# Kernel tuning notes

Hardware: AMD Instinct MI355X
Metric: run time of the kernel (lower is better)

The kernel has to match this reference:

```python
import jax, jax.numpy as jnp
import numpy as np

N_NODES = 100000
N_EDGES = 1600000

def _graph_conv(x, src, dst, W_rel, b_rel, W_root):
    # sum-aggregate source features at destination nodes (PyG GraphConv, aggr='add')
    agg = jax.ops.segment_sum(x[src], dst, num_segments=N_NODES)  # [N, Fin]
    return agg @ W_rel.T + b_rel + x @ W_root.T  # [N, Fout]

def setup_inputs() -> dict:
    key = jax.random.key(0)
    ks = jax.random.split(key, 10)
    x = jax.random.normal(ks[0], (N_NODES, 4), dtype=jnp.float32)
    edge_index = jax.random.randint(ks[1], (2, N_EDGES), 0, N_NODES, dtype=jnp.int32)
    def lin(k, fo, fi):
        return jax.random.normal(k, (fo, fi), dtype=jnp.float32) / np.sqrt(fi)
    return {
        "x": x,
        "edge_index": edge_index,
        "W1_rel": lin(ks[2], 128, 4),
        "b1": jax.random.normal(ks[3], (128,), dtype=jnp.float32) * 0.01,
        "W1_root": lin(ks[4], 128, 4),
        "W2_rel": lin(ks[5], 128, 128),
        "b2": jax.random.normal(ks[6], (128,), dtype=jnp.float32) * 0.01,
        "W2_root": lin(ks[7], 128, 128),
        "Wlin": lin(ks[8], 2, 128),
        "blin": jax.random.normal(ks[9], (2,), dtype=jnp.float32) * 0.01,
    }

def reference(x, edge_index, W1_rel, b1, W1_root, W2_rel, b2, W2_root, Wlin, blin):
    src, dst = edge_index[0], edge_index[1]
    h = jax.nn.relu(_graph_conv(x, src, dst, W1_rel, b1, W1_root))   # [N,128]
    h = jax.nn.relu(_graph_conv(h, src, dst, W2_rel, b2, W2_root))   # [N,128]
    # global_mean_pool with batch = zeros -> mean over all nodes, single graph
    g = jnp.mean(h, axis=0, keepdims=True)                           # [1,128]
    return g @ Wlin.T + blin                                         # [1,2]
```

## Files before the change

kernel.cpp:

```cpp
#include <hip/hip_runtime.h>
#include <cstddef>

#define N_NODES 100000
#define N_EDGES 1600000
#define NCHUNK32 3125
#define BUCK_SHIFT 6
#define BUCK_NODES 64
#define NBUCK 1563
#define EB_CAP 1536
#define BF_EDGES 4096
#define BF_BLOCKS ((N_EDGES + BF_EDGES - 1) / BF_EDGES)

typedef __attribute__((ext_vector_type(8))) short short8;
typedef __attribute__((ext_vector_type(4))) float f32x4;
typedef __attribute__((ext_vector_type(2))) float f32x2;

__device__ __forceinline__ unsigned pack_bf16x2(float a, float b) {
  unsigned ua = __float_as_uint(a); ua += 0x7FFFu + ((ua >> 16) & 1u);
  unsigned ub = __float_as_uint(b); ub += 0x7FFFu + ((ub >> 16) & 1u);
  return (ua >> 16) | (ub & 0xFFFF0000u);
}

__global__ __launch_bounds__(512) void k_init(int* __restrict__ bucket_cursor,
                                              float* __restrict__ gsum,
                                              const float* __restrict__ W2_rel,
                                              const float* __restrict__ W2_root,
                                              unsigned* __restrict__ wbuf) {
  int t = threadIdx.x;
  for (int b = t; b < NBUCK; b += 512) bucket_cursor[b] = b * EB_CAP;
  if (t < 128) gsum[t] = 0.0f;
#pragma unroll
  for (int i = 0; i < 8; ++i) {
    int e = t + i * 512;
    int L = e & 63, T = (e >> 6) & 7, K0 = e >> 9;
    int f = T * 16 + (L & 15);
    int k0 = K0 * 32 + ((L >> 4) << 3);
    const float* wsrc = (k0 < 128) ? (W2_rel + f * 128 + k0)
                                   : (W2_root + f * 128 + (k0 - 128));
    float4 w0 = *(const float4*)(wsrc);
    float4 w1 = *(const float4*)(wsrc + 4);
    unsigned* d = wbuf + e * 4;
    d[0] = pack_bf16x2(w0.x, w0.y);
    d[1] = pack_bf16x2(w0.z, w0.w);
    d[2] = pack_bf16x2(w1.x, w1.y);
    d[3] = pack_bf16x2(w1.z, w1.w);
  }
}

__global__ __launch_bounds__(256) void k_bfill(const int* __restrict__ src,
                                               const int* __restrict__ dst,
                                               int* __restrict__ bucket_cursor,
                                               unsigned* __restrict__ ebuf) {
  __shared__ int lh[NBUCK];
  __shared__ int sub_base[NBUCK];
  __shared__ int cur[NBUCK];
  int t = threadIdx.x;
  for (int b = t; b < NBUCK; b += 256) { lh[b] = 0; cur[b] = 0; }
  __syncthreads();
  int e0 = blockIdx.x * BF_EDGES;
  unsigned pk[16];
  int bk[16];
#pragma unroll
  for (int i = 0; i < 16; ++i) {
    int e = e0 + i * 256 + t;
    bk[i] = -1;
    if (e < N_EDGES) {
      int d = dst[e];
      int b = d >> BUCK_SHIFT;
      bk[i] = b;
      pk[i] = ((unsigned)(d & (BUCK_NODES - 1)) << 17) | (unsigned)src[e];
      atomicAdd(&lh[b], 1);
    }
  }
  __syncthreads();
  for (int b = t; b < NBUCK; b += 256)
    sub_base[b] = (lh[b] > 0) ? atomicAdd(&bucket_cursor[b], lh[b]) : 0;
  __syncthreads();
#pragma unroll
  for (int i = 0; i < 16; ++i) {
    if (bk[i] >= 0) {
      int pos = sub_base[bk[i]] + atomicAdd(&cur[bk[i]], 1);
      if (pos < (bk[i] + 1) * EB_CAP) ebuf[pos] = pk[i];
    }
  }
}

__global__ __launch_bounds__(256) void k_fill2(
    const unsigned* __restrict__ ebuf, const int* __restrict__ bucket_cursor,
    const float* __restrict__ x, const float* __restrict__ W1_rel,
    const float* __restrict__ b1, const float* __restrict__ W1_root,
    int* __restrict__ row_start, int* __restrict__ row_end,
    int* __restrict__ csr_src, unsigned* __restrict__ h1b,
    unsigned short* __restrict__ h1f8) {
  __shared__ int cnt[BUCK_NODES];
  __shared__ int start[BUCK_NODES];
  __shared__ float sagg[BUCK_NODES * 4];
  __shared__ float sx[BUCK_NODES * 4];
  __shared__ float sWa[8 * 128];
  __shared__ float sb1[128];
  int t = threadIdx.x;
  int b = blockIdx.x;
  int base = b * EB_CAP;
  int nb = bucket_cursor[b] - base;
  if (nb > EB_CAP) nb = EB_CAP;
  int n0 = b << BUCK_SHIFT;

  if (t < 128) {
    float4 wr = *(const float4*)(W1_rel + t * 4);
    float4 wo = *(const float4*)(W1_root + t * 4);
    sWa[0 * 128 + t] = wr.x; sWa[1 * 128 + t] = wr.y;
    sWa[2 * 128 + t] = wr.z; sWa[3 * 128 + t] = wr.w;
    sWa[4 * 128 + t] = wo.x; sWa[5 * 128 + t] = wo.y;
    sWa[6 * 128 + t] = wo.z; sWa[7 * 128 + t] = wo.w;
    sb1[t] = b1[t];
  }
  sagg[t] = 0.0f;
  if (t < BUCK_NODES) {
    cnt[t] = 0;
    float4 xv = make_float4(0.f, 0.f, 0.f, 0.f);
    if (n0 + t < N_NODES) xv = *(const float4*)(x + (size_t)(n0 + t) * 4);
    *(float4*)&sx[t * 4] = xv;
  }
  __syncthreads();

  for (int i = t; i < nb; i += 256) atomicAdd(&cnt[ebuf[base + i] >> 17], 1);
  __syncthreads();
  if (t == 0) {
    int s = 0;
#pragma unroll
    for (int j = 0; j < BUCK_NODES; ++j) { start[j] = s; s += cnt[j]; }
  }
  __syncthreads();
  if (t < BUCK_NODES) {
    if (n0 + t < N_NODES) row_start[n0 + t] = base + start[t];
    cnt[t] = start[t];
  }
  __syncthreads();
  for (int i = t; i < nb; i += 256) {
    unsigned e = ebuf[base + i];
    int dloc = e >> 17;
    int s = (int)(e & 0x1FFFFu);
    int p = atomicAdd(&cnt[dloc], 1);
    csr_src[base + p] = s;
    float4 v = *(const float4*)(x + (size_t)s * 4);
    atomicAdd(&sagg[dloc * 4 + 0], v.x);
    atomicAdd(&sagg[dloc * 4 + 1], v.y);
    atomicAdd(&sagg[dloc * 4 + 2], v.z);
    atomicAdd(&sagg[dloc * 4 + 3], v.w);
  }
  __syncthreads();
  if (t < BUCK_NODES && n0 + t < N_NODES) row_end[n0 + t] = base + cnt[t];

  for (int it = t; it < BUCK_NODES * 64; it += 256) {
    int nd = it >> 6;
    if (n0 + nd >= N_NODES) break;
    int fp = it & 63;
    int f = fp * 2;
    float4 a  = *(float4*)&sagg[nd * 4];
    float4 xv = *(float4*)&sx[nd * 4];
    float v0 = sb1[f]
        + a.x  * sWa[0 * 128 + f] + a.y  * sWa[1 * 128 + f]
        + a.z  * sWa[2 * 128 + f] + a.w  * sWa[3 * 128 + f]
        + xv.x * sWa[4 * 128 + f] + xv.y * sWa[5 * 128 + f]
        + xv.z * sWa[6 * 128 + f] + xv.w * sWa[7 * 128 + f];
    int f1 = f + 1;
    float v1 = sb1[f1]
        + a.x  * sWa[0 * 128 + f1] + a.y  * sWa[1 * 128 + f1]
        + a.z  * sWa[2 * 128 + f1] + a.w  * sWa[3 * 128 + f1]
        + xv.x * sWa[4 * 128 + f1] + xv.y * sWa[5 * 128 + f1]
        + xv.z * sWa[6 * 128 + f1] + xv.w * sWa[7 * 128 + f1];
    float r0 = fmaxf(v0, 0.f), r1 = fmaxf(v1, 0.f);
    size_t idx = (size_t)(n0 + nd) * 64 + fp;
    h1b[idx] = pack_bf16x2(r0, r1);
    h1f8[idx] = (unsigned short)__builtin_amdgcn_cvt_pk_fp8_f32(r0, r1, 0, false);
  }
}

__global__ __launch_bounds__(256) void k_pull128(
    const unsigned short* __restrict__ h1f8, const int* __restrict__ row_start,
    const int* __restrict__ row_end, const int* __restrict__ csr_src,
    unsigned* __restrict__ agg2b) {
  int w = (blockIdx.x * 256 + threadIdx.x) >> 6;
  if (w >= N_NODES) return;
  int lane = threadIdx.x & 63;
  int rs = row_start[w], re = row_end[w];
  float ax = 0.f, ay = 0.f;
  for (int chunk = rs; chunk < re; chunk += 64) {
    int nv = min(64, re - chunk);
    int sv = (chunk + lane < re) ? csr_src[chunk + lane] : 0;
    int j = 0;
    for (; j + 4 <= nv; j += 4) {
      int s0 = __shfl(sv, j);
      int s1 = __shfl(sv, j + 1);
      int s2 = __shfl(sv, j + 2);
      int s3 = __shfl(sv, j + 3);
      int u0 = h1f8[(size_t)s0 * 64 + lane];
      int u1 = h1f8[(size_t)s1 * 64 + lane];
      int u2 = h1f8[(size_t)s2 * 64 + lane];
      int u3 = h1f8[(size_t)s3 * 64 + lane];
      f32x2 d0 = __builtin_amdgcn_cvt_pk_f32_fp8(u0, false);
      f32x2 d1 = __builtin_amdgcn_cvt_pk_f32_fp8(u1, false);
      f32x2 d2 = __builtin_amdgcn_cvt_pk_f32_fp8(u2, false);
      f32x2 d3 = __builtin_amdgcn_cvt_pk_f32_fp8(u3, false);
      ax += d0.x + d1.x + d2.x + d3.x;
      ay += d0.y + d1.y + d2.y + d3.y;
    }
    for (; j < nv; ++j) {
      int s0 = __shfl(sv, j);
      int u0 = h1f8[(size_t)s0 * 64 + lane];
      f32x2 d0 = __builtin_amdgcn_cvt_pk_f32_fp8(u0, false);
      ax += d0.x; ay += d0.y;
    }
  }
  agg2b[(size_t)w * 64 + lane] = pack_bf16x2(ax, ay);
}

__global__ __launch_bounds__(256) void k_gemm_pool(
    const unsigned* __restrict__ agg2b_u, const unsigned* __restrict__ h1b_u,
    const unsigned* __restrict__ wbuf_u, const float* __restrict__ b2,
    float* __restrict__ gsum) {
  __shared__ float lgs[128];
  int t = threadIdx.x;
  if (t < 128) lgs[t] = 0.0f;
  __syncthreads();

  int lane = t & 63;
  int gw = blockIdx.x * 4 + (t >> 6);
  int lrow = lane & 15;
  int quad = lane >> 4;
  const unsigned short* agg2b = (const unsigned short*)agg2b_u;
  const unsigned short* h1b   = (const unsigned short*)h1b_u;
  const short8* wb = (const short8*)wbuf_u;

  float bias[8];
#pragma unroll
  for (int tt = 0; tt < 8; ++tt) bias[tt] = b2[tt * 16 + lrow];
  float csum[8] = {0.f, 0.f, 0.f, 0.f, 0.f, 0.f, 0.f, 0.f};

  if (gw < NCHUNK32) {
    int mbase = gw * 32;

    f32x4 acc[2][8];
#pragma unroll
    for (int mt = 0; mt < 2; ++mt)
#pragma unroll
      for (int tt = 0; tt < 8; ++tt) acc[mt][tt] = (f32x4){0.f, 0.f, 0.f, 0.f};

#pragma unroll
    for (int ks = 0; ks < 8; ++ks) {
      const unsigned short* abase = (ks < 4)
          ? (agg2b + ks * 32 + quad * 8)
          : (h1b + (ks - 4) * 32 + quad * 8);
      short8 afr[2];
#pragma unroll
      for (int mt = 0; mt < 2; ++mt)
        afr[mt] = *(const short8*)(abase + (size_t)(mbase + mt * 16 + lrow) * 128);
      short8 bfr[8];
#pragma unroll
      for (int tt = 0; tt < 8; ++tt) bfr[tt] = wb[(ks * 8 + tt) * 64 + lane];
#pragma unroll
      for (int mt = 0; mt < 2; ++mt)
#pragma unroll
        for (int tt = 0; tt < 8; ++tt)
          acc[mt][tt] = __builtin_amdgcn_mfma_f32_16x16x32_bf16(
              afr[mt], bfr[tt], acc[mt][tt], 0, 0, 0);
    }

#pragma unroll
    for (int mt = 0; mt < 2; ++mt) {
#pragma unroll
      for (int tt = 0; tt < 8; ++tt) {
        f32x4 v = acc[mt][tt];
        float s = fmaxf(v.x + bias[tt], 0.f) + fmaxf(v.y + bias[tt], 0.f)
                + fmaxf(v.z + bias[tt], 0.f) + fmaxf(v.w + bias[tt], 0.f);
        s += __shfl_xor(s, 16);
        s += __shfl_xor(s, 32);
        csum[tt] += s;
      }
    }
  }
  if (lane < 16) {
#pragma unroll
    for (int tt = 0; tt < 8; ++tt) atomicAdd(&lgs[tt * 16 + lane], csum[tt]);
  }
  __syncthreads();
  if (t < 128) atomicAdd(&gsum[t], lgs[t]);
}

__global__ void k_final(const float* __restrict__ gsum, const float* __restrict__ Wlin,
                        const float* __restrict__ blin, float* __restrict__ out) {
  int lane = threadIdx.x;
  float g0 = gsum[lane];
  float g1 = gsum[lane + 64];
  float s0 = g0 * Wlin[lane]       + g1 * Wlin[lane + 64];
  float s1 = g0 * Wlin[128 + lane] + g1 * Wlin[192 + lane];
#pragma unroll
  for (int off = 32; off > 0; off >>= 1) {
    s0 += __shfl_down(s0, off);
    s1 += __shfl_down(s1, off);
  }
  if (lane == 0) {
    const float inv = 1.0f / (float)N_NODES;
    out[0] = s0 * inv + blin[0];
    out[1] = s1 * inv + blin[1];
  }
}

extern "C" void kernel_launch(void* const* d_in, const int* in_sizes, int n_in,
                              void* d_out, int out_size, void* d_ws, size_t ws_size,
                              hipStream_t stream) {
  const float* x       = (const float*)d_in[0];
  const int*   ei      = (const int*)d_in[1];
  const float* W1_rel  = (const float*)d_in[2];
  const float* b1      = (const float*)d_in[3];
  const float* W1_root = (const float*)d_in[4];
  const float* W2_rel  = (const float*)d_in[5];
  const float* b2      = (const float*)d_in[6];
  const float* W2_root = (const float*)d_in[7];
  const float* Wlin    = (const float*)d_in[8];
  const float* blin    = (const float*)d_in[9];
  const int* src = ei;
  const int* dst = ei + N_EDGES;
  float* out = (float*)d_out;

  char* ws = (char*)d_ws;
  int*            row_start     = (int*)(ws);
  int*            row_end       = (int*)(ws + 400000);
  int*            bucket_cursor = (int*)(ws + 800000);
  float*          gsum          = (float*)(ws + 808192);
  unsigned*       wbuf          = (unsigned*)(ws + 808704);
  int*            csr_src       = (int*)(ws + 874240);
  unsigned*       ebuf          = (unsigned*)(ws + 10477312);
  unsigned*       h1b           = (unsigned*)(ws + 20080384);
  unsigned short* h1f8          = (unsigned short*)(ws + 45680384);
  unsigned*       agg2b         = (unsigned*)(ws + 58480384);

  k_init <<<1, 512, 0, stream>>>(bucket_cursor, gsum, W2_rel, W2_root, wbuf);
  k_bfill<<<BF_BLOCKS, 256, 0, stream>>>(src, dst, bucket_cursor, ebuf);
  k_fill2<<<NBUCK, 256, 0, stream>>>(ebuf, bucket_cursor, x, W1_rel, b1, W1_root,
                                     row_start, row_end, csr_src, h1b, h1f8);
  k_pull128<<<(N_NODES * 64 + 255) / 256, 256, 0, stream>>>(h1f8, row_start, row_end,
                                                            csr_src, agg2b);
  k_gemm_pool<<<(NCHUNK32 + 3) / 4, 256, 0, stream>>>(agg2b, h1b, wbuf, b2, gsum);
  k_final<<<1, 64, 0, stream>>>(gsum, Wlin, blin, out);
}
```

Baseline: 246.9 us.

## Drop bf16 h1 copy, use fp8 root operand, and restructure bucket fill

```diff
diff --git a/kernel.cpp b/kernel.cpp
--- a/kernel.cpp
+++ b/kernel.cpp
@@ -8,7 +8,7 @@
 #define BUCK_NODES 64
 #define NBUCK 1563
 #define EB_CAP 1536
-#define BF_EDGES 4096
+#define BF_EDGES 8192
 #define BF_BLOCKS ((N_EDGES + BF_EDGES - 1) / BF_EDGES)
 
 typedef __attribute__((ext_vector_type(8))) short short8;
@@ -47,7 +47,7 @@
   }
 }
 
-__global__ __launch_bounds__(256) void k_bfill(const int* __restrict__ src,
+__global__ __launch_bounds__(512) void k_bfill(const int* __restrict__ src,
                                                const int* __restrict__ dst,
                                                int* __restrict__ bucket_cursor,
                                                unsigned* __restrict__ ebuf) {
@@ -55,14 +55,14 @@
   __shared__ int sub_base[NBUCK];
   __shared__ int cur[NBUCK];
   int t = threadIdx.x;
-  for (int b = t; b < NBUCK; b += 256) { lh[b] = 0; cur[b] = 0; }
+  for (int b = t; b < NBUCK; b += 512) { lh[b] = 0; cur[b] = 0; }
   __syncthreads();
   int e0 = blockIdx.x * BF_EDGES;
   unsigned pk[16];
   int bk[16];
 #pragma unroll
   for (int i = 0; i < 16; ++i) {
-    int e = e0 + i * 256 + t;
+    int e = e0 + i * 512 + t;
     bk[i] = -1;
     if (e < N_EDGES) {
       int d = dst[e];
@@ -73,7 +73,7 @@
     }
   }
   __syncthreads();
-  for (int b = t; b < NBUCK; b += 256)
+  for (int b = t; b < NBUCK; b += 512)
     sub_base[b] = (lh[b] > 0) ? atomicAdd(&bucket_cursor[b], lh[b]) : 0;
   __syncthreads();
 #pragma unroll
@@ -90,8 +90,7 @@
     const float* __restrict__ x, const float* __restrict__ W1_rel,
     const float* __restrict__ b1, const float* __restrict__ W1_root,
     int* __restrict__ row_start, int* __restrict__ row_end,
-    int* __restrict__ csr_src, unsigned* __restrict__ h1b,
-    unsigned short* __restrict__ h1f8) {
+    int* __restrict__ csr_src, unsigned short* __restrict__ h1f8) {
   __shared__ int cnt[BUCK_NODES];
   __shared__ int start[BUCK_NODES];
   __shared__ float sagg[BUCK_NODES * 4];
@@ -114,7 +113,6 @@
     sWa[6 * 128 + t] = wo.z; sWa[7 * 128 + t] = wo.w;
     sb1[t] = b1[t];
   }
-  sagg[t] = 0.0f;
   if (t < BUCK_NODES) {
     cnt[t] = 0;
     float4 xv = make_float4(0.f, 0.f, 0.f, 0.f);
@@ -125,31 +123,47 @@
 
   for (int i = t; i < nb; i += 256) atomicAdd(&cnt[ebuf[base + i] >> 17], 1);
   __syncthreads();
-  if (t == 0) {
-    int s = 0;
-#pragma unroll
-    for (int j = 0; j < BUCK_NODES; ++j) { start[j] = s; s += cnt[j]; }
-  }
-  __syncthreads();
-  if (t < BUCK_NODES) {
-    if (n0 + t < N_NODES) row_start[n0 + t] = base + start[t];
-    cnt[t] = start[t];
+  if (t < 64) {
+    int v = cnt[t];
+    int incl = v;
+#pragma unroll
+    for (int off = 1; off < 64; off <<= 1) {
+      int nvv = __shfl_up(incl, off);
+      if (t >= off) incl += nvv;
+    }
+    int excl = incl - v;
+    start[t] = excl;
+    cnt[t] = excl;
+    if (n0 + t < N_NODES) row_start[n0 + t] = base + excl;
   }
   __syncthreads();
   for (int i = t; i < nb; i += 256) {
     unsigned e = ebuf[base + i];
-    int dloc = e >> 17;
-    int s = (int)(e & 0x1FFFFu);
-    int p = atomicAdd(&cnt[dloc], 1);
-    csr_src[base + p] = s;
-    float4 v = *(const float4*)(x + (size_t)s * 4);
-    atomicAdd(&sagg[dloc * 4 + 0], v.x);
-    atomicAdd(&sagg[dloc * 4 + 1], v.y);
-    atomicAdd(&sagg[dloc * 4 + 2], v.z);
-    atomicAdd(&sagg[dloc * 4 + 3], v.w);
-  }
-  __syncthreads();
-  if (t < BUCK_NODES && n0 + t < N_NODES) row_end[n0 + t] = base + cnt[t];
+    int p = atomicAdd(&cnt[e >> 17], 1);
+    csr_src[base + p] = (int)(e & 0x1FFFFu);
+  }
+  __syncthreads();
+  {
+    int nd = t >> 2, sub = t & 3;
+    int rs = base + start[nd];
+    int re = base + cnt[nd];
+    float4 acc = make_float4(0.f, 0.f, 0.f, 0.f);
+    for (int i = rs + sub; i < re; i += 4) {
+      int s = csr_src[i];
+      float4 v = *(const float4*)(x + (size_t)s * 4);
+      acc.x += v.x; acc.y += v.y; acc.z += v.z; acc.w += v.w;
+    }
+#pragma unroll
+    for (int off = 1; off < 4; off <<= 1) {
+      acc.x += __shfl_xor(acc.x, off);
+      acc.y += __shfl_xor(acc.y, off);
+      acc.z += __shfl_xor(acc.z, off);
+      acc.w += __shfl_xor(acc.w, off);
+    }
+    if (sub == 0) *(float4*)&sagg[nd * 4] = acc;
+    if (t < 64 && n0 + t < N_NODES) row_end[n0 + t] = base + cnt[t];
+  }
+  __syncthreads();
 
   for (int it = t; it < BUCK_NODES * 64; it += 256) {
     int nd = it >> 6;
@@ -170,9 +184,8 @@
         + xv.x * sWa[4 * 128 + f1] + xv.y * sWa[5 * 128 + f1]
         + xv.z * sWa[6 * 128 + f1] + xv.w * sWa[7 * 128 + f1];
     float r0 = fmaxf(v0, 0.f), r1 = fmaxf(v1, 0.f);
-    size_t idx = (size_t)(n0 + nd) * 64 + fp;
-    h1b[idx] = pack_bf16x2(r0, r1);
-    h1f8[idx] = (unsigned short)__builtin_amdgcn_cvt_pk_fp8_f32(r0, r1, 0, false);
+    h1f8[(size_t)(n0 + nd) * 64 + fp] =
+        (unsigned short)__builtin_amdgcn_cvt_pk_fp8_f32(r0, r1, 0, false);
   }
 }
 
@@ -216,7 +229,7 @@
 }
 
 __global__ __launch_bounds__(256) void k_gemm_pool(
-    const unsigned* __restrict__ agg2b_u, const unsigned* __restrict__ h1b_u,
+    const unsigned* __restrict__ agg2b_u, const unsigned short* __restrict__ h1f8,
     const unsigned* __restrict__ wbuf_u, const float* __restrict__ b2,
     float* __restrict__ gsum) {
   __shared__ float lgs[128];
@@ -229,7 +242,7 @@
   int lrow = lane & 15;
   int quad = lane >> 4;
   const unsigned short* agg2b = (const unsigned short*)agg2b_u;
-  const unsigned short* h1b   = (const unsigned short*)h1b_u;
+  const unsigned char* h8 = (const unsigned char*)h1f8;
   const short8* wb = (const short8*)wbuf_u;
 
   float bias[8];
@@ -247,14 +260,41 @@
       for (int tt = 0; tt < 8; ++tt) acc[mt][tt] = (f32x4){0.f, 0.f, 0.f, 0.f};
 
 #pragma unroll
-    for (int ks = 0; ks < 8; ++ks) {
-      const unsigned short* abase = (ks < 4)
-          ? (agg2b + ks * 32 + quad * 8)
-          : (h1b + (ks - 4) * 32 + quad * 8);
+    for (int ks = 0; ks < 4; ++ks) {
+      const unsigned short* abase = agg2b + ks * 32 + quad * 8;
       short8 afr[2];
 #pragma unroll
       for (int mt = 0; mt < 2; ++mt)
         afr[mt] = *(const short8*)(abase + (size_t)(mbase + mt * 16 + lrow) * 128);
+      short8 bfr[8];
+#pragma unroll
+      for (int tt = 0; tt < 8; ++tt) bfr[tt] = wb[(ks * 8 + tt) * 64 + lane];
+#pragma unroll
+      for (int mt = 0; mt < 2; ++mt)
+#pragma unroll
+        for (int tt = 0; tt < 8; ++tt)
+          acc[mt][tt] = __builtin_amdgcn_mfma_f32_16x16x32_bf16(
+              afr[mt], bfr[tt], acc[mt][tt], 0, 0, 0);
+    }
+#pragma unroll
+    for (int ks = 4; ks < 8; ++ks) {
+      short8 afr[2];
+#pragma unroll
+      for (int mt = 0; mt < 2; ++mt) {
+        const uint2* ap = (const uint2*)(h8 + (size_t)(mbase + mt * 16 + lrow) * 128
+                                         + (ks - 4) * 32 + quad * 8);
+        uint2 u = *ap;
+        f32x2 a0 = __builtin_amdgcn_cvt_pk_f32_fp8((int)u.x, false);
+        f32x2 a1 = __builtin_amdgcn_cvt_pk_f32_fp8((int)u.x, true);
+        f32x2 a2 = __builtin_amdgcn_cvt_pk_f32_fp8((int)u.y, false);
+        f32x2 a3 = __builtin_amdgcn_cvt_pk_f32_fp8((int)u.y, true);
+        unsigned q0 = pack_bf16x2(a0.x, a0.y);
+        unsigned q1 = pack_bf16x2(a1.x, a1.y);
+        unsigned q2 = pack_bf16x2(a2.x, a2.y);
+        unsigned q3 = pack_bf16x2(a3.x, a3.y);
+        unsigned q[4] = {q0, q1, q2, q3};
+        afr[mt] = *(short8*)q;
+      }
       short8 bfr[8];
 #pragma unroll
       for (int tt = 0; tt < 8; ++tt) bfr[tt] = wb[(ks * 8 + tt) * 64 + lane];
@@ -331,16 +371,15 @@
   unsigned*       wbuf          = (unsigned*)(ws + 808704);
   int*            csr_src       = (int*)(ws + 874240);
   unsigned*       ebuf          = (unsigned*)(ws + 10477312);
-  unsigned*       h1b           = (unsigned*)(ws + 20080384);
-  unsigned short* h1f8          = (unsigned short*)(ws + 45680384);
-  unsigned*       agg2b         = (unsigned*)(ws + 58480384);
+  unsigned short* h1f8          = (unsigned short*)(ws + 20080384);
+  unsigned*       agg2b         = (unsigned*)(ws + 32880384);
 
   k_init <<<1, 512, 0, stream>>>(bucket_cursor, gsum, W2_rel, W2_root, wbuf);
-  k_bfill<<<BF_BLOCKS, 256, 0, stream>>>(src, dst, bucket_cursor, ebuf);
+  k_bfill<<<BF_BLOCKS, 512, 0, stream>>>(src, dst, bucket_cursor, ebuf);
   k_fill2<<<NBUCK, 256, 0, stream>>>(ebuf, bucket_cursor, x, W1_rel, b1, W1_root,
-                                     row_start, row_end, csr_src, h1b, h1f8);
+                                     row_start, row_end, csr_src, h1f8);
   k_pull128<<<(N_NODES * 64 + 255) / 256, 256, 0, stream>>>(h1f8, row_start, row_end,
                                                             csr_src, agg2b);
-  k_gemm_pool<<<(NCHUNK32 + 3) / 4, 256, 0, stream>>>(agg2b, h1b, wbuf, b2, gsum);
+  k_gemm_pool<<<(NCHUNK32 + 3) / 4, 256, 0, stream>>>(agg2b, h1f8, wbuf, b2, gsum);
   k_final<<<1, 64, 0, stream>>>(gsum, Wlin, blin, out);
 }
```

New measurement: 212.6 us. 13.9% less time.
